# Performance work log

Hardware: AMD Instinct MI355X
Metric: run time of the kernel (lower is better)

Reference implementation:

```python
import jax, jax.numpy as jnp
import numpy as np

MASK_NEG = -1e9

def setup_inputs() -> dict:
    key = jax.random.key(0)
    kq, kk, kv, km = jax.random.split(key, 4)
    B, S, D = 16, 2048, 64
    query = jax.random.normal(kq, (B, S, D), dtype=jnp.float32)
    key_t = jax.random.normal(kk, (B, S, D), dtype=jnp.float32)
    value = jax.random.normal(kv, (B, S, D), dtype=jnp.float32)
    mask = jax.random.randint(km, (B, 1, S), 0, 2, dtype=jnp.int32)
    return {"query": query, "key": key_t, "value": value, "mask": mask}

def reference(query, key, value, mask):
    d = query.shape[-1]
    # scores: [B, S, S]
    scores = jnp.einsum("bqd,bkd->bqk", query, key) / jnp.sqrt(jnp.asarray(d, query.dtype))
    scores = jnp.where(mask == 0, jnp.asarray(MASK_NEG, scores.dtype), scores)
    p_attn = jax.nn.softmax(scores, axis=-1)
    out = jnp.einsum("bqk,bkd->bqd", p_attn, value)
    return out, p_attn
```

## Files before the change

### kernel.cpp

```cpp
#include <hip/hip_runtime.h>
#include <hip/hip_bf16.h>

#define BN 16
#define SN 2048
#define DN 64
#define QB 16
#define NWAVE 8
#define KSEG 256
#define NCH 8

#define SC_L2E 0.18033688011112042f
#define BI_L2E 11.541560327111707f

typedef __attribute__((ext_vector_type(8))) short bf16x8;
typedef __attribute__((ext_vector_type(4))) short bf16x4;
typedef __attribute__((ext_vector_type(4))) float f32x4;
typedef __attribute__((ext_vector_type(4))) int   i32x4;
typedef __attribute__((ext_vector_type(2))) unsigned u32x2;
typedef __attribute__((ext_vector_type(4))) unsigned u32x4;

static __device__ __forceinline__ short f2bf(float f) {
    __hip_bfloat16 h = __float2bfloat16(f);
    union { __hip_bfloat16 h; short s; } u; u.h = h;
    return u.s;
}
static __device__ __forceinline__ float uf(unsigned u) {
    union { unsigned u; float f; } v; v.u = u;
    return v.f;
}
static __device__ __forceinline__ unsigned pk2(float lo, float hi) {
    return ((unsigned)(unsigned short)f2bf(lo)) |
           (((unsigned)(unsigned short)f2bf(hi)) << 16);
}
static __device__ __forceinline__ float fast_exp2(float x) {
#if __has_builtin(__builtin_amdgcn_exp2f)
    return __builtin_amdgcn_exp2f(x);
#else
    return exp2f(x);
#endif
}

__global__ __launch_bounds__(256)
void prep_kv(const float* __restrict__ K, const float* __restrict__ V,
             const int* __restrict__ M,
             short* __restrict__ Kf, short* __restrict__ Vf, float* __restrict__ Mf)
{
    __shared__ short vt[64][72];
    const int b   = blockIdx.x >> 5;
    const int s0  = (blockIdx.x & 31) << 6;
    const int cg0 = s0 >> 5;
    const int tid = threadIdx.x;
    const int sr = tid >> 4;
    const int dc = (tid & 15) << 2;
    #pragma unroll
    for (int i = 0; i < 4; ++i) {
        const int s = sr + i * 16;
        f32x4 vv = *(const f32x4*)(V + ((size_t)b * SN + s0 + s) * DN + dc);
        bf16x4 v4;
        #pragma unroll
        for (int j = 0; j < 4; ++j) v4[j] = f2bf(vv[j]);
        *(bf16x4*)&vt[s][dc] = v4;
    }
    if (tid < 64) {
        const int m = M[(size_t)b * SN + s0 + tid];
        Mf[(size_t)b * SN + s0 + tid] = m ? -BI_L2E : -1e9f;
    }
    __syncthreads();

    #pragma unroll
    for (int r = 0; r < 2; ++r) {
        const int o   = tid + (r << 8);
        const int h   = o >> 8;
        const int s   = (o >> 6) & 3;
        const int l2  = o & 63;
        const int lq2 = l2 & 15, lg2 = l2 >> 4;
        const int srow = s0 + h * 32 + ((s >> 1) & 1) * 16 + lq2;
        const int scol = (s & 1) * 32 + lg2 * 8;
        const float* kp = K + ((size_t)b * SN + srow) * DN + scol;
        f32x4 x = *(const f32x4*)kp;
        f32x4 y = *(const f32x4*)(kp + 4);
        bf16x8 kv;
        #pragma unroll
        for (int j = 0; j < 4; ++j) { kv[j] = f2bf(x[j]); kv[4 + j] = f2bf(y[j]); }
        *(bf16x8*)(Kf + (size_t)(((b * 64 + cg0 + h) * 4 + s) * 512 + l2 * 8)) = kv;
    }
    #pragma unroll
    for (int r = 0; r < 2; ++r) {
        const int o   = tid + (r << 8);
        const int h   = o >> 8;
        const int nt  = (o >> 6) & 3;
        const int l2  = o & 63;
        const int lq2 = l2 & 15, lg2 = l2 >> 4;
        const int d   = nt * 16 + lq2;
        bf16x8 w;
        #pragma unroll
        for (int j = 0; j < 4; ++j) {
            w[j]     = vt[h * 32 + 4 * lg2 + j][d];
            w[4 + j] = vt[h * 32 + 16 + 4 * lg2 + j][d];
        }
        *(bf16x8*)(Vf + (size_t)(((b * 64 + cg0 + h) * 4 + nt) * 512 + l2 * 8)) = w;
    }
}

template <int PRE>
__global__ __launch_bounds__(512, 3)
void attn_fused(const float* __restrict__ Q, const float* __restrict__ K,
                const float* __restrict__ V, const int* __restrict__ M,
                const short* __restrict__ Kf, const short* __restrict__ Vf,
                const float* __restrict__ Mf, float* __restrict__ out)
{
    __shared__ float obuf[NWAVE * QB * DN];
    __shared__ float lred[NWAVE * QB];
    __shared__ float lfin[QB];

    const int tid = threadIdx.x;
    const int wv = tid >> 6, ln = tid & 63;
    const int lq = ln & 15, lg = ln >> 4;

    const int lb = ((blockIdx.x & 7) << 8) | (blockIdx.x >> 3);
    const int bb = lb >> 7;
    const int q0 = (lb & 127) << 4;

    const float* Qb = Q + ((size_t)bb * SN + q0) * DN;
    float* out_o = out + ((size_t)bb * SN + q0) * DN;
    float* out_p = out + (size_t)BN * SN * DN + ((size_t)bb * SN + q0) * SN;

    u32x4* stash = (u32x4*)obuf + (wv << 8) + ln;

    bf16x8 qf0, qf1;
    {
        const float* src = Qb + lq * DN + lg * 8;
        f32x4 a = *(const f32x4*)src;
        f32x4 b = *(const f32x4*)(src + 4);
        f32x4 c = *(const f32x4*)(src + 32);
        f32x4 d = *(const f32x4*)(src + 36);
        #pragma unroll
        for (int j = 0; j < 4; ++j) {
            qf0[j] = f2bf(a[j]); qf0[4 + j] = f2bf(b[j]);
            qf1[j] = f2bf(c[j]); qf1[4 + j] = f2bf(d[j]);
        }
    }

    const int k0 = wv * KSEG;
    const int cgb = bb * 64 + wv * NCH;
    const short* kfp = Kf + (size_t)cgb * 2048 + ln * 8;
    const short* vfp = Vf + (size_t)cgb * 2048 + ln * 8;
    const float* fp  = Mf + (size_t)bb * SN + k0 + 4 * lg;
    const int*   Mb  = M + (size_t)bb * SN;
    const float* Kb  = K + (size_t)bb * SN * DN;
    const float* Vb  = V + (size_t)bb * SN * DN;

    unsigned pk_lo[4][4];
    float ls0 = 0.f, ls1 = 0.f;

    #pragma unroll
    for (int c = 0; c < NCH; ++c) {
        bf16x8 kf0, kf1, kf2, kf3;
        f32x4 b0, b1;
        if constexpr (PRE) {
            kf0 = *(const bf16x8*)(kfp + c * 2048);
            kf1 = *(const bf16x8*)(kfp + c * 2048 + 512);
            kf2 = *(const bf16x8*)(kfp + c * 2048 + 1024);
            kf3 = *(const bf16x8*)(kfp + c * 2048 + 1536);
            b0 = *(const f32x4*)(fp + c * 32);
            b1 = *(const f32x4*)(fp + c * 32 + 16);
        } else {
            const float* ks = Kb + (size_t)(k0 + c * 32 + lq) * DN + lg * 8;
            #pragma unroll
            for (int j = 0; j < 8; ++j) {
                kf0[j] = f2bf(ks[j]);            kf1[j] = f2bf(ks[32 + j]);
                kf2[j] = f2bf(ks[16 * DN + j]);  kf3[j] = f2bf(ks[16 * DN + 32 + j]);
            }
            const i32x4 mv0 = *(const i32x4*)(Mb + k0 + c * 32 + 4 * lg);
            const i32x4 mv1 = *(const i32x4*)(Mb + k0 + c * 32 + 16 + 4 * lg);
            #pragma unroll
            for (int r = 0; r < 4; ++r) {
                b0[r] = mv0[r] ? -BI_L2E : -1e9f;
                b1[r] = mv1[r] ? -BI_L2E : -1e9f;
            }
        }
        f32x4 a0 = {0.f, 0.f, 0.f, 0.f}, a1 = {0.f, 0.f, 0.f, 0.f};
        __builtin_amdgcn_s_setprio(1);
        a0 = __builtin_amdgcn_mfma_f32_16x16x32_bf16(kf0, qf0, a0, 0, 0, 0);
        a0 = __builtin_amdgcn_mfma_f32_16x16x32_bf16(kf1, qf1, a0, 0, 0, 0);
        a1 = __builtin_amdgcn_mfma_f32_16x16x32_bf16(kf2, qf0, a1, 0, 0, 0);
        a1 = __builtin_amdgcn_mfma_f32_16x16x32_bf16(kf3, qf1, a1, 0, 0, 0);

        float p0[4], p1[4];
        #pragma unroll
        for (int r = 0; r < 4; ++r) {
            p0[r] = fast_exp2(fmaf(a0[r], SC_L2E, b0[r]));
            p1[r] = fast_exp2(fmaf(a1[r], SC_L2E, b1[r]));
            ls0 += p0[r];
            ls1 += p1[r];
        }
        u32x4 w;
        w[0] = pk2(p0[0], p0[1]); w[1] = pk2(p0[2], p0[3]);
        w[2] = pk2(p1[0], p1[1]); w[3] = pk2(p1[2], p1[3]);
        __builtin_amdgcn_s_setprio(0);
        if (c < 4) {
            pk_lo[c][0] = w[0]; pk_lo[c][1] = w[1];
            pk_lo[c][2] = w[2]; pk_lo[c][3] = w[3];
        } else {
            stash[(c - 4) << 6] = w;
        }
    }

    bf16x8 pv0[4], pv1[4];
    if constexpr (PRE) {
        pv0[0] = *(const bf16x8*)(vfp);
        pv0[1] = *(const bf16x8*)(vfp + 512);
        pv0[2] = *(const bf16x8*)(vfp + 1024);
        pv0[3] = *(const bf16x8*)(vfp + 1536);
        pv1[0] = *(const bf16x8*)(vfp + 2048);
        pv1[1] = *(const bf16x8*)(vfp + 2048 + 512);
        pv1[2] = *(const bf16x8*)(vfp + 2048 + 1024);
        pv1[3] = *(const bf16x8*)(vfp + 2048 + 1536);
    }

    float lsum = ls0 + ls1;
    lsum += __shfl_xor(lsum, 16);
    lsum += __shfl_xor(lsum, 32);
    if (lg == 0) lred[wv * QB + lq] = lsum;
    __syncthreads();
    if (tid < QB) {
        float l = 0.f;
        #pragma unroll
        for (int w = 0; w < NWAVE; ++w) l += lred[w * QB + tid];
        lfin[tid] = 1.f / l;
    }
    __syncthreads();

    f32x4 oacc[4];
    #pragma unroll
    for (int nt = 0; nt < 4; ++nt) oacc[nt] = (f32x4){0.f, 0.f, 0.f, 0.f};

    #pragma unroll
    for (int c = 0; c < NCH; ++c) {
        union { unsigned u[4]; u32x4 w; bf16x8 v; } pa;
        if (c < 4) {
            pa.u[0] = pk_lo[c][0]; pa.u[1] = pk_lo[c][1];
            pa.u[2] = pk_lo[c][2]; pa.u[3] = pk_lo[c][3];
        } else {
            pa.w = stash[(c - 4) << 6];
        }

        bf16x8 vf0, vf1, vf2, vf3;
        if constexpr (PRE) {
            if (c == 0) { vf0 = pv0[0]; vf1 = pv0[1]; vf2 = pv0[2]; vf3 = pv0[3]; }
            else if (c == 1) { vf0 = pv1[0]; vf1 = pv1[1]; vf2 = pv1[2]; vf3 = pv1[3]; }
            else {
                vf0 = *(const bf16x8*)(vfp + c * 2048);
                vf1 = *(const bf16x8*)(vfp + c * 2048 + 512);
                vf2 = *(const bf16x8*)(vfp + c * 2048 + 1024);
                vf3 = *(const bf16x8*)(vfp + c * 2048 + 1536);
            }
        } else {
            #pragma unroll
            for (int j = 0; j < 4; ++j) {
                const float* va = Vb + (size_t)(k0 + c * 32 + 4 * lg + j) * DN + lq;
                const float* vb = Vb + (size_t)(k0 + c * 32 + 16 + 4 * lg + j) * DN + lq;
                vf0[j] = f2bf(va[0]);  vf0[4 + j] = f2bf(vb[0]);
                vf1[j] = f2bf(va[16]); vf1[4 + j] = f2bf(vb[16]);
                vf2[j] = f2bf(va[32]); vf2[4 + j] = f2bf(vb[32]);
                vf3[j] = f2bf(va[48]); vf3[4 + j] = f2bf(vb[48]);
            }
        }
        __builtin_amdgcn_s_setprio(1);
        oacc[0] = __builtin_amdgcn_mfma_f32_16x16x32_bf16(pa.v, vf0, oacc[0], 0, 0, 0);
        oacc[1] = __builtin_amdgcn_mfma_f32_16x16x32_bf16(pa.v, vf1, oacc[1], 0, 0, 0);
        oacc[2] = __builtin_amdgcn_mfma_f32_16x16x32_bf16(pa.v, vf2, oacc[2], 0, 0, 0);
        oacc[3] = __builtin_amdgcn_mfma_f32_16x16x32_bf16(pa.v, vf3, oacc[3], 0, 0, 0);
        __builtin_amdgcn_s_setprio(0);
    }

    {
        const char* wb = (const char*)obuf + (wv << 12);
        const int i    = ln & 31;
        const int c_sl = i >> 3;
        const int j    = i & 7;
        const int soff = c_sl * 1024 + ((j & 3) * 16) * 16 + (j >> 2) * 8;
        const int rsel = ln >> 5;

        #pragma unroll
        for (int it = 0; it < 8; ++it) {
            const int row = 2 * it + rsel;
            const u32x2 w = *(const u32x2*)(wb + soff + row * 16);
            const float rl = lfin[row];
            f32x4 o;
            o[0] = uf(w[0] << 16) * rl;  o[1] = uf(w[0] & 0xffff0000u) * rl;
            o[2] = uf(w[1] << 16) * rl;  o[3] = uf(w[1] & 0xffff0000u) * rl;
            __builtin_nontemporal_store(o,
                (f32x4*)(out_p + (size_t)row * SN + k0 + 128 + i * 4));
        }
        #pragma unroll
        for (int c = 0; c < 4; ++c) {
            u32x4 w;
            w[0] = pk_lo[c][0]; w[1] = pk_lo[c][1];
            w[2] = pk_lo[c][2]; w[3] = pk_lo[c][3];
            stash[c << 6] = w;
        }
        #pragma unroll
        for (int it = 0; it < 8; ++it) {
            const int row = 2 * it + rsel;
            const u32x2 w = *(const u32x2*)(wb + soff + row * 16);
            const float rl = lfin[row];
            f32x4 o;
            o[0] = uf(w[0] << 16) * rl;  o[1] = uf(w[0] & 0xffff0000u) * rl;
            o[2] = uf(w[1] << 16) * rl;  o[3] = uf(w[1] & 0xffff0000u) * rl;
            __builtin_nontemporal_store(o,
                (f32x4*)(out_p + (size_t)row * SN + k0 + i * 4));
        }
    }

    #pragma unroll
    for (int nt = 0; nt < 4; ++nt) {
        #pragma unroll
        for (int r = 0; r < 4; ++r)
            obuf[(wv * QB + 4 * lg + r) * DN + nt * 16 + lq] = oacc[nt][r];
    }
    __syncthreads();
    #pragma unroll
    for (int i = 0; i < 2; ++i) {
        const int idx = tid + i * 512;
        const int q = idx >> 6, d = idx & 63;
        float v = 0.f;
        #pragma unroll
        for (int w = 0; w < NWAVE; ++w) v += obuf[(w * QB + q) * DN + d];
        __builtin_nontemporal_store(v * lfin[q], &out_o[(size_t)q * DN + d]);
    }
}

extern "C" void kernel_launch(void* const* d_in, const int* in_sizes, int n_in,
                              void* d_out, int out_size, void* d_ws, size_t ws_size,
                              hipStream_t stream) {
    const float* Q = (const float*)d_in[0];
    const float* K = (const float*)d_in[1];
    const float* V = (const float*)d_in[2];
    const int*   M = (const int*)d_in[3];
    float* out = (float*)d_out;

    const size_t szKf = (size_t)BN * 64 * 4 * 512 * sizeof(short);
    const size_t szVf = szKf;
    const size_t szMf = (size_t)BN * SN * sizeof(float);
    const size_t need = szKf + szVf + szMf;

    dim3 block(512);
    dim3 grid(BN * (SN / QB));
    if (ws_size >= need) {
        short* Kf = (short*)d_ws;
        short* Vf = (short*)((char*)d_ws + szKf);
        float* Mf = (float*)((char*)d_ws + szKf + szVf);
        prep_kv<<<dim3(BN * (SN / 64)), dim3(256), 0, stream>>>(K, V, M, Kf, Vf, Mf);
        attn_fused<1><<<grid, block, 0, stream>>>(Q, K, V, M, Kf, Vf, Mf, out);
    } else {
        attn_fused<0><<<grid, block, 0, stream>>>(Q, K, V, M, nullptr, nullptr, nullptr, out);
    }
}
```

Measured before the change: 81.78 us.

## Interleave normalized P stores with PV MFMA chunks

```diff
diff --git a/kernel.cpp b/kernel.cpp
--- a/kernel.cpp
+++ b/kernel.cpp
@@ -206,16 +206,16 @@
         }
     }
 
-    bf16x8 pv0[4], pv1[4];
+    bf16x8 pv4[4], pv5[4];
     if constexpr (PRE) {
-        pv0[0] = *(const bf16x8*)(vfp);
-        pv0[1] = *(const bf16x8*)(vfp + 512);
-        pv0[2] = *(const bf16x8*)(vfp + 1024);
-        pv0[3] = *(const bf16x8*)(vfp + 1536);
-        pv1[0] = *(const bf16x8*)(vfp + 2048);
-        pv1[1] = *(const bf16x8*)(vfp + 2048 + 512);
-        pv1[2] = *(const bf16x8*)(vfp + 2048 + 1024);
-        pv1[3] = *(const bf16x8*)(vfp + 2048 + 1536);
+        pv4[0] = *(const bf16x8*)(vfp + 4 * 2048);
+        pv4[1] = *(const bf16x8*)(vfp + 4 * 2048 + 512);
+        pv4[2] = *(const bf16x8*)(vfp + 4 * 2048 + 1024);
+        pv4[3] = *(const bf16x8*)(vfp + 4 * 2048 + 1536);
+        pv5[0] = *(const bf16x8*)(vfp + 5 * 2048);
+        pv5[1] = *(const bf16x8*)(vfp + 5 * 2048 + 512);
+        pv5[2] = *(const bf16x8*)(vfp + 5 * 2048 + 1024);
+        pv5[3] = *(const bf16x8*)(vfp + 5 * 2048 + 1536);
     }
 
     float lsum = ls0 + ls1;
@@ -235,20 +235,33 @@
     #pragma unroll
     for (int nt = 0; nt < 4; ++nt) oacc[nt] = (f32x4){0.f, 0.f, 0.f, 0.f};
 
-    #pragma unroll
-    for (int c = 0; c < NCH; ++c) {
+    const char* wb = (const char*)obuf + (wv << 12);
+    const int di   = ln & 31;
+    const int dj   = di & 7;
+    const int soff = (di >> 3) * 1024 + ((dj & 3) * 16) * 16 + (dj >> 2) * 8;
+    const int rsel = ln >> 5;
+
+    #pragma unroll
+    for (int c = 4; c < 8; ++c) {
         union { unsigned u[4]; u32x4 w; bf16x8 v; } pa;
-        if (c < 4) {
-            pa.u[0] = pk_lo[c][0]; pa.u[1] = pk_lo[c][1];
-            pa.u[2] = pk_lo[c][2]; pa.u[3] = pk_lo[c][3];
-        } else {
-            pa.w = stash[(c - 4) << 6];
+        pa.w = stash[(c - 4) << 6];
+
+        #pragma unroll
+        for (int t = 0; t < 2; ++t) {
+            const int row = 2 * (2 * (c - 4) + t) + rsel;
+            const u32x2 w = *(const u32x2*)(wb + soff + row * 16);
+            const float rl = lfin[row];
+            f32x4 o;
+            o[0] = uf(w[0] << 16) * rl;  o[1] = uf(w[0] & 0xffff0000u) * rl;
+            o[2] = uf(w[1] << 16) * rl;  o[3] = uf(w[1] & 0xffff0000u) * rl;
+            __builtin_nontemporal_store(o,
+                (f32x4*)(out_p + (size_t)row * SN + k0 + 128 + di * 4));
         }
 
         bf16x8 vf0, vf1, vf2, vf3;
         if constexpr (PRE) {
-            if (c == 0) { vf0 = pv0[0]; vf1 = pv0[1]; vf2 = pv0[2]; vf3 = pv0[3]; }
-            else if (c == 1) { vf0 = pv1[0]; vf1 = pv1[1]; vf2 = pv1[2]; vf3 = pv1[3]; }
+            if (c == 4) { vf0 = pv4[0]; vf1 = pv4[1]; vf2 = pv4[2]; vf3 = pv4[3]; }
+            else if (c == 5) { vf0 = pv5[0]; vf1 = pv5[1]; vf2 = pv5[2]; vf3 = pv5[3]; }
             else {
                 vf0 = *(const bf16x8*)(vfp + c * 2048);
                 vf1 = *(const bf16x8*)(vfp + c * 2048 + 512);
@@ -274,43 +287,55 @@
         __builtin_amdgcn_s_setprio(0);
     }
 
-    {
-        const char* wb = (const char*)obuf + (wv << 12);
-        const int i    = ln & 31;
-        const int c_sl = i >> 3;
-        const int j    = i & 7;
-        const int soff = c_sl * 1024 + ((j & 3) * 16) * 16 + (j >> 2) * 8;
-        const int rsel = ln >> 5;
-
-        #pragma unroll
-        for (int it = 0; it < 8; ++it) {
-            const int row = 2 * it + rsel;
+    #pragma unroll
+    for (int c = 0; c < 4; ++c) {
+        u32x4 w;
+        w[0] = pk_lo[c][0]; w[1] = pk_lo[c][1];
+        w[2] = pk_lo[c][2]; w[3] = pk_lo[c][3];
+        stash[c << 6] = w;
+    }
+
+    #pragma unroll
+    for (int c = 0; c < 4; ++c) {
+        union { unsigned u[4]; bf16x8 v; } pa;
+        pa.u[0] = pk_lo[c][0]; pa.u[1] = pk_lo[c][1];
+        pa.u[2] = pk_lo[c][2]; pa.u[3] = pk_lo[c][3];
+
+        #pragma unroll
+        for (int t = 0; t < 2; ++t) {
+            const int row = 2 * (2 * c + t) + rsel;
             const u32x2 w = *(const u32x2*)(wb + soff + row * 16);
             const float rl = lfin[row];
             f32x4 o;
             o[0] = uf(w[0] << 16) * rl;  o[1] = uf(w[0] & 0xffff0000u) * rl;
             o[2] = uf(w[1] << 16) * rl;  o[3] = uf(w[1] & 0xffff0000u) * rl;
             __builtin_nontemporal_store(o,
-                (f32x4*)(out_p + (size_t)row * SN + k0 + 128 + i * 4));
-        }
-        #pragma unroll
-        for (int c = 0; c < 4; ++c) {
-            u32x4 w;
-            w[0] = pk_lo[c][0]; w[1] = pk_lo[c][1];
-            w[2] = pk_lo[c][2]; w[3] = pk_lo[c][3];
-            stash[c << 6] = w;
-        }
-        #pragma unroll
-        for (int it = 0; it < 8; ++it) {
-            const int row = 2 * it + rsel;
-            const u32x2 w = *(const u32x2*)(wb + soff + row * 16);
-            const float rl = lfin[row];
-            f32x4 o;
-            o[0] = uf(w[0] << 16) * rl;  o[1] = uf(w[0] & 0xffff0000u) * rl;
-            o[2] = uf(w[1] << 16) * rl;  o[3] = uf(w[1] & 0xffff0000u) * rl;
-            __builtin_nontemporal_store(o,
-                (f32x4*)(out_p + (size_t)row * SN + k0 + i * 4));
-        }
+                (f32x4*)(out_p + (size_t)row * SN + k0 + di * 4));
+        }
+
+        bf16x8 vf0, vf1, vf2, vf3;
+        if constexpr (PRE) {
+            vf0 = *(const bf16x8*)(vfp + c * 2048);
+            vf1 = *(const bf16x8*)(vfp + c * 2048 + 512);
+            vf2 = *(const bf16x8*)(vfp + c * 2048 + 1024);
+            vf3 = *(const bf16x8*)(vfp + c * 2048 + 1536);
+        } else {
+            #pragma unroll
+            for (int j = 0; j < 4; ++j) {
+                const float* va = Vb + (size_t)(k0 + c * 32 + 4 * lg + j) * DN + lq;
+                const float* vb = Vb + (size_t)(k0 + c * 32 + 16 + 4 * lg + j) * DN + lq;
+                vf0[j] = f2bf(va[0]);  vf0[4 + j] = f2bf(vb[0]);
+                vf1[j] = f2bf(va[16]); vf1[4 + j] = f2bf(vb[16]);
+                vf2[j] = f2bf(va[32]); vf2[4 + j] = f2bf(vb[32]);
+                vf3[j] = f2bf(va[48]); vf3[4 + j] = f2bf(vb[48]);
+            }
+        }
+        __builtin_amdgcn_s_setprio(1);
+        oacc[0] = __builtin_amdgcn_mfma_f32_16x16x32_bf16(pa.v, vf0, oacc[0], 0, 0, 0);
+        oacc[1] = __builtin_amdgcn_mfma_f32_16x16x32_bf16(pa.v, vf1, oacc[1], 0, 0, 0);
+        oacc[2] = __builtin_amdgcn_mfma_f32_16x16x32_bf16(pa.v, vf2, oacc[2], 0, 0, 0);
+        oacc[3] = __builtin_amdgcn_mfma_f32_16x16x32_bf16(pa.v, vf3, oacc[3], 0, 0, 0);
+        __builtin_amdgcn_s_setprio(0);
     }
 
     #pragma unroll
```

New measurement: 76.91 us (median of 2 runs). 1.06x faster.
